# Performance work log

Hardware: AMD Instinct MI355X
Metric: run time of the kernel (lower is better)

## Reference

```python
import jax, jax.numpy as jnp
from jax import lax
import numpy as np

FL = 7      # filter_length (odd so each decomposition level preserves L)
LEVEL = 3
T = 5       # time_points
C = 64      # channels
HID = 64    # ODE hidden width (== C so ODE state shape is preserved)
TD = 16     # time embedding dim
REG = 0.01  # DyWAN reg_factor


def _gelu(x):
    return jax.nn.gelu(x, approximate=False)  # torch nn.GELU default = exact


def _conv1d(x, w, b, pad):
    # x [B,Cin,L], w [Cout,Cin,K] -> [B,Cout,L'] (cross-correlation, as torch)
    out = lax.conv_general_dilated(x, w, (1,), [(pad, pad)],
                                   dimension_numbers=('NCH', 'OIH', 'NCH'))
    return out + b[None, :, None]


def _dywan(x, w1, b1, wg1, bg1, wg2, bg2):
    # DyWAN_Pro: global stats -> dynamic lo/hi filters + regularizers
    stat = x.mean(-1)                                  # AdaptiveAvgPool1d(1)+Flatten
    h = _gelu(stat @ w1.T + b1)
    h = _gelu(h @ wg1.T + bg1)
    f = h @ wg2.T + bg2                                # [B, 2*FL]
    lo, hi = f[:, :FL], f[:, FL:]
    # smoothness: conv1d with kernel [-1,1], zero pad 1 -> xp[l+1]-xp[l]
    lp = jnp.pad(lo, ((0, 0), (1, 1)))
    lo_smooth = jnp.abs(lp[:, 1:] - lp[:, :-1]).mean()
    lo_n = lo / (jnp.linalg.norm(lo, axis=1, keepdims=True) + 1e-8)
    shift_loss = 0.0
    for s in (1, 2, 3):
        sh = jnp.roll(lo_n, s, axis=1)
        shift_loss = shift_loss + jnp.abs(lo_n[:, :, None] * sh[:, None, :]).mean()
    amp_loss = jnp.abs((lo_n ** 2).sum(1) - 1.0).mean()
    ortho = REG * (shift_loss + amp_loss)
    return lo, hi, ortho + lo_smooth * 0.1


def _batch_filter_conv(ap, filt):
    # per-sample depthwise conv: ap [B,C,L], filt [B,FL] -> [B,C,L]
    B, Ch, L = ap.shape
    pad = (FL - 1) // 2
    xp = jnp.pad(ap, ((0, 0), (0, 0), (pad, pad)), mode='edge')  # replicate pad
    xp = xp.reshape(1, B * Ch, L + 2 * pad)
    k = jnp.repeat(filt[:, None, :], Ch, axis=1).reshape(B * Ch, 1, FL)
    out = lax.conv_general_dilated(xp, k, (1,), 'VALID',
                                   dimension_numbers=('NCH', 'OIH', 'NCH'),
                                   feature_group_count=B * Ch)
    return out.reshape(B, Ch, -1)[..., :L]


def _adaptive_time_grid(sig):
    g = jnp.abs(jnp.diff(sig, axis=-1))                          # [B,C,L-1]
    gp = jnp.pad(g, ((0, 0), (0, 0), (2, 2)))                    # avg_pool1d k=5 pad=2
    cs = jnp.pad(jnp.cumsum(gp, axis=-1), ((0, 0), (0, 0), (1, 0)))
    inten = (cs[..., 5:] - cs[..., :-5]) / 5.0                   # [B,C,L-1]
    mn, mx = inten.min(), inten.max()
    td = jnp.where(mx - mn < 1e-8, 0.5,
                   (inten - mn) / (mx - mn + 1e-30) * 0.9 + 0.1)
    tg = jnp.concatenate([jnp.zeros_like(td[..., :1]),
                          jnp.cumsum(td[..., :-1], -1)], -1)     # time_grid
    tg = tg / jnp.maximum(tg.max(), 1e-12)
    idx = np.linspace(0, td.shape[-1] - 1, T).astype(np.int64)   # static indices
    return tg[..., idx].mean((0, 1))                             # [T], increasing


def reference(x, dy_w1, dy_b1, dy_wg1, dy_bg1, dy_wg2, dy_bg2,
              ode_c1w, ode_c1b, ode_c2w, ode_c2b, ode_wt, ode_bt,
              ode_wm, ode_bm, ode_emb,
              gate_w, gate_b, attn1_w, attn1_b, attn2_w, attn2_b):
    # ---- multi-level dynamic wavelet decomposition ----
    coeffs = [x]
    approx = x
    ortho = jnp.float32(0.0)
    for _ in range(LEVEL):
        lo, hi, ortho = _dywan(approx, dy_w1, dy_b1, dy_wg1, dy_bg1, dy_wg2, dy_bg2)
        new_approx = _batch_filter_conv(approx, lo)
        detail = _batch_filter_conv(approx, hi)
        coeffs.append(detail)
        approx = new_approx
    coeffs[0] = approx

    # ---- per-scale ODE evolution: RK4 over the adaptive time grid ----
    def ode_f(t, y, lvl):
        h = _conv1d(y, ode_c1w[lvl], ode_c1b[lvl], 1)
        h = _gelu(h)
        h = _conv1d(h, ode_c2w[lvl], ode_c2b[lvl], 1)
        temb = jax.nn.silu(ode_wt[lvl][:, 0] * t + ode_bt[lvl])   # [TD]
        gb = ode_wm[lvl] @ temb + ode_bm[lvl]                     # [2*HID]
        gamma, beta = gb[:HID], gb[HID:]
        se = ode_emb[lvl, lvl]                                    # scale embedding
        mod = h * (1.0 + gamma + se)[None, :, None] + beta[None, :, None]
        return jax.nn.silu(mod) - 0.1 * y                         # PhysicsActivation

    evolved = []
    for lvl in range(LEVEL + 1):
        c = coeffs[lvl]
        ts = _adaptive_time_grid(c)
        y = c
        for j in range(T - 1):
            t0, t1 = ts[j], ts[j + 1]
            dt = t1 - t0
            k1 = ode_f(t0, y, lvl)
            k2 = ode_f(t0 + dt / 2, y + dt / 2 * k1, lvl)
            k3 = ode_f(t0 + dt / 2, y + dt / 2 * k2, lvl)
            k4 = ode_f(t1, y + dt * k3, lvl)
            y = y + dt / 6 * (k1 + 2 * k2 + 2 * k3 + k4)
        e_in = jnp.mean(c ** 2, axis=(1, 2), keepdims=True)
        e_out = jnp.mean(y ** 2, axis=(1, 2), keepdims=True)
        evolved.append(y * jnp.sqrt(e_in / (e_out + 1e-8)))       # energy constraint

    # ---- gated cross-scale fusion ----
    current = evolved[0]
    yh = evolved[1:]
    enhanced = []
    for i in range(LEVEL - 1, -1, -1):
        detail = yh[i]
        if i < LEVEL - 1:
            a = _gelu(_conv1d(current, attn1_w[i], attn1_b[i], 0))
            a = jax.nn.sigmoid(_conv1d(a, attn2_w[i], attn2_b[i], 0))
            detail = detail * a + detail
        gate = jax.nn.sigmoid(_conv1d(current, gate_w[i], gate_b[i], 1))
        current = current + gate * detail
        enhanced.append(detail)
    enhanced.reverse()
    out = jnp.stack([current] + enhanced, axis=0)   # [LEVEL+1, B, C, L] = (yl, yh...)
    return out, ortho


def setup_inputs() -> dict:
    key = jax.random.key(0)
    ks = jax.random.split(key, 16)
    B, L = 8, 2048

    def rn(k, shape, sc=0.1):
        return jax.random.normal(k, shape, dtype=jnp.float32) * sc

    return {
        'x': jax.random.normal(ks[0], (B, C, L), dtype=jnp.float32),
        'dy_w1': rn(ks[1], (HID, C)),
        'dy_b1': jnp.zeros((HID,), jnp.float32),
        'dy_wg1': rn(ks[2], (2 * HID, HID)),
        'dy_bg1': jnp.zeros((2 * HID,), jnp.float32),
        'dy_wg2': rn(ks[3], (2 * FL, 2 * HID)),
        'dy_bg2': rn(ks[4], (2 * FL,), 0.1),
        'ode_c1w': rn(ks[5], (LEVEL + 1, HID, C, 3)),
        'ode_c1b': jnp.zeros((LEVEL + 1, HID), jnp.float32),
        'ode_c2w': rn(ks[6], (LEVEL + 1, HID, HID, 3)),
        'ode_c2b': jnp.zeros((LEVEL + 1, HID), jnp.float32),
        'ode_wt': rn(ks[7], (LEVEL + 1, TD, 1)),
        'ode_bt': jnp.zeros((LEVEL + 1, TD), jnp.float32),
        'ode_wm': rn(ks[8], (LEVEL + 1, 2 * HID, TD)),
        'ode_bm': jnp.zeros((LEVEL + 1, 2 * HID), jnp.float32),
        'ode_emb': rn(ks[9], (LEVEL + 1, 8, HID)),
        'gate_w': rn(ks[10], (LEVEL, C, C, 3)),
        'gate_b': jnp.zeros((LEVEL, C), jnp.float32),
        'attn1_w': rn(ks[11], (LEVEL - 1, C // 4, C, 1)),
        'attn1_b': jnp.zeros((LEVEL - 1, C // 4), jnp.float32),
        'attn2_w': rn(ks[12], (LEVEL - 1, C, C // 4, 1)),
        'attn2_b': jnp.zeros((LEVEL - 1, C), jnp.float32),
    }
```

## Files before the change

### kernel.cpp

```cpp
#include <hip/hip_runtime.h>
#include <math.h>

#define LSEQ 2048
#define NB 8
#define NCH 64
#define NTOT (NB*NCH*LSEQ)
#define NROWS (NB*NCH)

typedef __attribute__((ext_vector_type(8))) short short8;
typedef __attribute__((ext_vector_type(4))) float float4v;

__device__ __forceinline__ float geluf(float x){
    return 0.5f*x*(1.0f+erff(x*0.70710678118654752f));
}
__device__ __forceinline__ float siluf(float x){
    return x/(1.0f+expf(-x));
}
__device__ __forceinline__ float sigf(float x){
    return 1.0f/(1.0f+expf(-x));
}
__device__ __forceinline__ unsigned short f2bf(float f){
    unsigned u=__float_as_uint(f);
    u += 0x7fffu + ((u>>16)&1u);
    return (unsigned short)(u>>16);
}
__device__ __forceinline__ float bf2f(unsigned h){
    return __uint_as_float((h&0xffffu)<<16);
}

__global__ __launch_bounds__(256) void wtrans_kernel(const float* __restrict__ w,
                                                     float* __restrict__ wt){
    int idx = blockIdx.x*256 + threadIdx.x;
    int j = idx >> 6, co = idx & 63;
    wt[idx] = w[co*192 + j];
}

__global__ __launch_bounds__(256) void wprep_kernel(const float* __restrict__ c1w,
                                                    const float* __restrict__ c2w,
                                                    short* __restrict__ WB){
    int idx = blockIdx.x*256 + threadIdx.x;
    if (idx >= 196608) return;
    int ci  = idx & 63;
    int co  = (idx>>6) & 63;
    int tap = (idx>>12) % 3;
    int st  = (idx/(3<<12)) & 1;
    int lvl = idx/(6<<12);
    const float* src = (st==0? c1w : c2w);
    float w = src[(size_t)lvl*12288 + co*192 + ci*3 + tap];
    unsigned short hi = f2bf(w);
    float lo = w - bf2f(hi);
    size_t base = ((((size_t)(lvl*2+st)*2+0)*3+tap)*64+co)*64+ci;
    size_t basl = ((((size_t)(lvl*2+st)*2+1)*3+tap)*64+co)*64+ci;
    WB[base] = (short)hi;
    WB[basl] = (short)f2bf(lo);
}

__global__ __launch_bounds__(256) void stat_kernel(const float* __restrict__ in,
                                                   float* __restrict__ stat){
    int r = blockIdx.x, tid = threadIdx.x;
    const float* p = in + (size_t)r*LSEQ;
    float acc = 0.f;
    for (int i=tid;i<LSEQ;i+=256) acc += p[i];
    for (int o=32;o>0;o>>=1) acc += __shfl_down(acc,o,64);
    __shared__ float red[4];
    if ((tid&63)==0) red[tid>>6]=acc;
    __syncthreads();
    if (tid==0) stat[r] = (red[0]+red[1]+red[2]+red[3])*(1.0f/LSEQ);
}

__global__ __launch_bounds__(256) void dywan_kernel(
    const float* __restrict__ stat,
    const float* __restrict__ w1, const float* __restrict__ b1,
    const float* __restrict__ wg1, const float* __restrict__ bg1,
    const float* __restrict__ wg2, const float* __restrict__ bg2,
    float* __restrict__ lo_out, float* __restrict__ hi_out,
    float* __restrict__ ortho_out)
{
    __shared__ float st[512];
    __shared__ float h1s[512];
    __shared__ float h2s[1024];
    __shared__ float fs[112];
    int tid = threadIdx.x;
    for (int i=tid;i<512;i+=256) st[i]=stat[i];
    __syncthreads();
    for (int idx=tid; idx<512; idx+=256){
        int b=idx>>6, j=idx&63;
        float acc=b1[j];
        const float* W=w1+j*64;
        for (int i=0;i<64;i++) acc += st[b*64+i]*W[i];
        h1s[idx]=geluf(acc);
    }
    __syncthreads();
    for (int idx=tid; idx<1024; idx+=256){
        int b=idx>>7, j=idx&127;
        float acc=bg1[j];
        const float* W=wg1+j*64;
        for (int i=0;i<64;i++) acc += h1s[b*64+i]*W[i];
        h2s[idx]=geluf(acc);
    }
    __syncthreads();
    if (tid<112){
        int b=tid/14, j=tid-b*14;
        float acc=bg2[j];
        const float* W=wg2+j*128;
        for (int i=0;i<128;i++) acc += h2s[b*128+i]*W[i];
        fs[tid]=acc;
    }
    __syncthreads();
    if (tid<56){
        int b=tid/7, k=tid-b*7;
        lo_out[tid]=fs[b*14+k];
        hi_out[tid]=fs[b*14+7+k];
    }
    if (tid==0){
        float smooth=0.f, shiftsum=0.f, ampsum=0.f;
        for (int b=0;b<8;b++){
            const float* l = fs + b*14;
            float prev=0.f, nrm=0.f;
            for (int k=0;k<7;k++){ smooth += fabsf(l[k]-prev); prev=l[k]; nrm += l[k]*l[k]; }
            smooth += fabsf(prev);
            float denom = sqrtf(nrm) + 1e-8f;
            float sabs=0.f, s2=0.f;
            for (int k=0;k<7;k++){ float v=l[k]/denom; sabs+=fabsf(v); s2+=v*v; }
            shiftsum += sabs*sabs;
            ampsum += fabsf(s2-1.0f);
        }
        smooth *= (1.0f/64.0f);
        float shift = 3.0f*shiftsum/(8.0f*49.0f);
        float amp = ampsum*(1.0f/8.0f);
        *ortho_out = 0.01f*(shift+amp) + 0.1f*smooth;
    }
}

__global__ __launch_bounds__(256) void filt_kernel(
    const float* __restrict__ ap, const float* __restrict__ lo,
    const float* __restrict__ hi, float* __restrict__ na,
    float* __restrict__ det)
{
    int r = blockIdx.y, l0 = blockIdx.x*256, tid = threadIdx.x;
    int b = r>>6;
    __shared__ float s[262];
    __shared__ float fl[7], fh[7];
    for (int idx=tid; idx<262; idx+=256){
        int l = l0+idx-3;
        l = min(max(l,0),LSEQ-1);
        s[idx]=ap[(size_t)r*LSEQ+l];
    }
    if (tid<7) fl[tid]=lo[b*7+tid];
    else if (tid<14) fh[tid-7]=hi[b*7+tid-7];
    __syncthreads();
    float a=0.f, d=0.f;
    #pragma unroll
    for (int k=0;k<7;k++){ float v=s[tid+k]; a+=v*fl[k]; d+=v*fh[k]; }
    na[(size_t)r*LSEQ+l0+tid]=a;
    det[(size_t)r*LSEQ+l0+tid]=d;
}

__global__ __launch_bounds__(256) void tg_pass1(const float* __restrict__ CB,
                                                float* __restrict__ rowstats){
    __shared__ float sh[2048];
    __shared__ float red[28];
    int r = blockIdx.x, lvl = blockIdx.y, tid = threadIdx.x;
    const float* s = CB + (size_t)lvl*NTOT + (size_t)r*LSEQ;
    float* rso = rowstats + (size_t)(lvl*NROWS+r)*8;
    for (int i=tid;i<2048;i+=256) sh[i]=s[i];
    __syncthreads();
    float ssq=0.f;
    for (int i=tid;i<2048;i+=256){ float v=sh[i]; ssq+=v*v; }
    float mn=1e30f, mx=-1e30f, s0=0.f,s1=0.f,s2=0.f,s3=0.f;
    for (int j=tid;j<2047;j+=256){
        int k0 = (j-2>0)? j-2:0;
        int k1 = (j+2<2046)? j+2:2046;
        float acc=0.f;
        for (int k=k0;k<=k1;k++) acc += fabsf(sh[k+1]-sh[k]);
        float inten = acc*0.2f;
        mn=fminf(mn,inten); mx=fmaxf(mx,inten);
        if (j<511)  s0+=inten;
        if (j<1023) s1+=inten;
        if (j<1534) s2+=inten;
        if (j<2046) s3+=inten;
    }
    float vals[7]={mn,mx,s0,s1,s2,s3,ssq};
    for (int o=32;o>0;o>>=1){
        vals[0]=fminf(vals[0],__shfl_down(vals[0],o,64));
        vals[1]=fmaxf(vals[1],__shfl_down(vals[1],o,64));
        vals[2]+=__shfl_down(vals[2],o,64);
        vals[3]+=__shfl_down(vals[3],o,64);
        vals[4]+=__shfl_down(vals[4],o,64);
        vals[5]+=__shfl_down(vals[5],o,64);
        vals[6]+=__shfl_down(vals[6],o,64);
    }
    int lane=tid&63, w=tid>>6;
    if (lane==0) for (int q=0;q<7;q++) red[w*7+q]=vals[q];
    __syncthreads();
    if (tid==0){
        rso[0]=fminf(fminf(red[0],red[7]),fminf(red[14],red[21]));
        rso[1]=fmaxf(fmaxf(red[1],red[8]),fmaxf(red[15],red[22]));
        rso[2]=red[2]+red[9]+red[16]+red[23];
        rso[3]=red[3]+red[10]+red[17]+red[24];
        rso[4]=red[4]+red[11]+red[18]+red[25];
        rso[5]=red[5]+red[12]+red[19]+red[26];
        rso[6]=red[6]+red[13]+red[20]+red[27];
    }
}

__global__ __launch_bounds__(256) void tg_finalize(
    const float* __restrict__ rowstats,
    const float* __restrict__ wt, const float* __restrict__ bt,
    const float* __restrict__ wm, const float* __restrict__ bm,
    const float* __restrict__ emb,
    float* __restrict__ ts_out, float* __restrict__ modsc,
    float* __restrict__ modbi, float* __restrict__ ein,
    float* __restrict__ eout)
{
    int tid=threadIdx.x;
    const int lvl=blockIdx.x;
    const float* rs = rowstats + (size_t)lvl*NROWS*8;
    __shared__ float red[28];
    __shared__ float stv[9];
    __shared__ float temb[144];
    float mn=1e30f,mx=-1e30f,a0=0.f,a1=0.f,a2=0.f,a3=0.f,m3=-1e30f;
    for (int r=tid;r<512;r+=256){
        mn=fminf(mn,rs[r*8+0]); mx=fmaxf(mx,rs[r*8+1]);
        a0+=rs[r*8+2]; a1+=rs[r*8+3]; a2+=rs[r*8+4]; a3+=rs[r*8+5];
        m3=fmaxf(m3,rs[r*8+5]);
    }
    float vals[7]={mn,mx,a0,a1,a2,a3,m3};
    for (int o=32;o>0;o>>=1){
        vals[0]=fminf(vals[0],__shfl_down(vals[0],o,64));
        vals[1]=fmaxf(vals[1],__shfl_down(vals[1],o,64));
        vals[2]+=__shfl_down(vals[2],o,64);
        vals[3]+=__shfl_down(vals[3],o,64);
        vals[4]+=__shfl_down(vals[4],o,64);
        vals[5]+=__shfl_down(vals[5],o,64);
        vals[6]=fmaxf(vals[6],__shfl_down(vals[6],o,64));
    }
    int lane=tid&63, w=tid>>6;
    if (lane==0) for (int q=0;q<7;q++) red[w*7+q]=vals[q];
    if (tid<8){
        float e=0.f;
        for (int c=0;c<64;c++) e += rs[(tid*64+c)*8+6];
        ein[lvl*8+tid]=e*(1.0f/131072.0f);
        eout[lvl*8+tid]=0.f;
    }
    __syncthreads();
    if (tid==0){
        float mnv=fminf(fminf(red[0],red[7]),fminf(red[14],red[21]));
        float mxv=fmaxf(fmaxf(red[1],red[8]),fmaxf(red[15],red[22]));
        float s0=red[2]+red[9]+red[16]+red[23];
        float s1=red[3]+red[10]+red[17]+red[24];
        float s2=red[4]+red[11]+red[18]+red[25];
        float s3=red[5]+red[12]+red[19]+red[26];
        float m3v=fmaxf(fmaxf(red[6],red[13]),fmaxf(red[20],red[27]));
        const float idxs[5]={0.f,511.f,1023.f,1534.f,2046.f};
        float tsv[5];
        if (mxv-mnv < 1e-8f){
            for (int k=0;k<5;k++) tsv[k]=idxs[k]/2046.0f;
        } else {
            float a = 0.9f/(mxv-mnv+1e-30f);
            float bb = 0.1f - a*mnv;
            float gmax = a*m3v + bb*2046.0f;
            float sums[5]={0.f,s0,s1,s2,s3};
            tsv[0]=0.f;
            for (int k=1;k<5;k++)
                tsv[k]=(a*(sums[k]*(1.0f/512.0f)) + bb*idxs[k])/gmax;
        }
        for (int k=0;k<5;k++){ ts_out[lvl*8+k]=tsv[k]; stv[2*k]=tsv[k]; }
        for (int k=0;k<4;k++) stv[2*k+1]=tsv[k] + 0.5f*(tsv[k+1]-tsv[k]);
    }
    __syncthreads();
    if (tid<144){
        int m=tid>>4, i=tid&15;
        float z = wt[lvl*16+i]*stv[m] + bt[lvl*16+i];
        temb[tid]=siluf(z);
    }
    __syncthreads();
    for (int idx=tid; idx<1152; idx+=256){
        int m=idx>>7, c=idx&127;
        float g=bm[lvl*128+c];
        const float* W=wm+(size_t)(lvl*128+c)*16;
        const float* te=temb+m*16;
        for (int i=0;i<16;i++) g += W[i]*te[i];
        if (c<64) modsc[lvl*576+m*64+c]=1.0f+g+emb[(lvl*8+lvl)*64+c];
        else      modbi[lvl*576+m*64+(c-64)]=g;
    }
}

__global__ __launch_bounds__(256) void ode_eval_all(
    const float* __restrict__ yinB, const unsigned* __restrict__ kprevB,
    unsigned* __restrict__ koutB, unsigned* __restrict__ accB,
    float* __restrict__ youtB,
    const short* __restrict__ WB, const float* __restrict__ c1bB,
    const float* __restrict__ c2bB,
    const float* __restrict__ modscB, const float* __restrict__ modbiB,
    const float* __restrict__ tsB, float* __restrict__ eoutB,
    int step, int eval, int do_energy)
{
    __shared__ unsigned yTh[68][36];
    __shared__ unsigned yTl[68][36];
    __shared__ unsigned hTh[66][36];
    __shared__ float red[4];
    const int tid=threadIdx.x;
    const int lvl=blockIdx.z;
    const int b=blockIdx.y;
    const int l0=blockIdx.x*64;
    const size_t loff=(size_t)lvl*NTOT;
    const size_t loffP=(size_t)lvl*(NTOT/2);
    const float* yin = yinB + loff;
    const unsigned* kprev = kprevB + loffP;
    unsigned* kout = koutB + loffP;
    unsigned* acc = accB + loffP;
    float* yout = youtB + loff;
    const float dt = tsB[lvl*8+step+1]-tsB[lvl*8+step];
    const float alpha=(eval==0)?0.f:((eval==3)?dt:0.5f*dt);
    const int tslot=2*step+((eval==0)?0:((eval==3)?2:1));
    const int wv=tid>>6, lane=tid&63;
    const int n=lane&15, quad=lane>>4;
    const int m0=wv*16;

    #pragma unroll
    for (int pass=0; pass<2; pass++){
        int r = pass*64 + lane;
        if (r < 68){
            int l = l0 - 2 + r;
            bool ok = (l>=0 && l<LSEQ);
            #pragma unroll
            for (int qq=0; qq<8; qq++){
                int q = wv*8 + qq;
                float v0=0.f, v1=0.f;
                if (ok){
                    size_t g0=(size_t)(b*64+2*q)*LSEQ+l;
                    v0=yin[g0]; v1=yin[g0+LSEQ];
                    if (eval!=0){
                        unsigned ku = kprev[((size_t)(b*32+q))*LSEQ + l];
                        v0 += alpha*bf2f(ku);
                        v1 += alpha*bf2f(ku>>16);
                    }
                }
                unsigned short h0=f2bf(v0), h1=f2bf(v1);
                yTh[r][q] = (unsigned)h0 | ((unsigned)h1<<16);
                yTl[r][q] = (unsigned)f2bf(v0-bf2f(h0)) | ((unsigned)f2bf(v1-bf2f(h1))<<16);
            }
        }
    }
    __syncthreads();

    {
        const short* W1 = WB + (size_t)(lvl*2+0)*2*3*4096;
        short8 A[3][2][2];
        #pragma unroll
        for (int tap=0;tap<3;tap++)
            #pragma unroll
            for (int ks=0;ks<2;ks++)
                #pragma unroll
                for (int hl=0;hl<2;hl++)
                    A[tap][ks][hl] = *(const short8*)(W1 + (((size_t)hl*3+tap)*64 + (m0+n))*64 + ks*32 + quad*8);
        float bia[4];
        #pragma unroll
        for (int reg=0;reg<4;reg++) bia[reg]=c1bB[lvl*64 + m0 + quad*4 + reg];
        const int q0=(m0>>1)+quad*2;
        for (int nt=0; nt<5; nt++){
            float4v d = {bia[0],bia[1],bia[2],bia[3]};
            #pragma unroll
            for (int tap=0;tap<3;tap++){
                int rr = 16*nt + n + tap;
                rr = (rr>67)? 67 : rr;
                const unsigned* ph=&yTh[rr][0];
                const unsigned* pl=&yTl[rr][0];
                #pragma unroll
                for (int ks=0;ks<2;ks++){
                    short8 bh = *(const short8*)(ph + ks*16 + quad*4);
                    short8 bl = *(const short8*)(pl + ks*16 + quad*4);
                    d = __builtin_amdgcn_mfma_f32_16x16x32_bf16(A[tap][ks][0], bh, d, 0,0,0);
                    d = __builtin_amdgcn_mfma_f32_16x16x32_bf16(A[tap][ks][0], bl, d, 0,0,0);
                    d = __builtin_amdgcn_mfma_f32_16x16x32_bf16(A[tap][ks][1], bh, d, 0,0,0);
                }
            }
            if (nt<4 || n<2){
                int rh = 16*nt + n;
                int hpos = l0 - 1 + rh;
                bool okh = (hpos>=0 && hpos<LSEQ);
                float h0 = okh? geluf(d[0]) : 0.f;
                float h1 = okh? geluf(d[1]) : 0.f;
                float h2 = okh? geluf(d[2]) : 0.f;
                float h3 = okh? geluf(d[3]) : 0.f;
                hTh[rh][q0]   = (unsigned)f2bf(h0) | ((unsigned)f2bf(h1)<<16);
                hTh[rh][q0+1] = (unsigned)f2bf(h2) | ((unsigned)f2bf(h3)<<16);
            }
        }
    }
    __syncthreads();

    float esum=0.f;
    {
        const short* W2 = WB + (size_t)(lvl*2+1)*2*3*4096;
        short8 A[3][2][2];
        #pragma unroll
        for (int tap=0;tap<3;tap++)
            #pragma unroll
            for (int ks=0;ks<2;ks++)
                #pragma unroll
                for (int hl=0;hl<2;hl++)
                    A[tap][ks][hl] = *(const short8*)(W2 + (((size_t)hl*3+tap)*64 + (m0+n))*64 + ks*32 + quad*8);
        float bib[4], sc[4], bi2[4];
        #pragma unroll
        for (int reg=0;reg<4;reg++){
            int co = m0 + quad*4 + reg;
            bib[reg]=c2bB[lvl*64+co];
            sc[reg]=modscB[lvl*576+tslot*64+co];
            bi2[reg]=modbiB[lvl*576+tslot*64+co];
        }
        const float dt6 = dt/6.0f;
        const int qy0=(m0+quad*4)>>1;
        for (int nt=0; nt<4; nt++){
            float4v d = {bib[0],bib[1],bib[2],bib[3]};
            #pragma unroll
            for (int tap=0;tap<3;tap++){
                const int rr = 16*nt + n + tap;
                const unsigned* ph=&hTh[rr][0];
                #pragma unroll
                for (int ks=0;ks<2;ks++){
                    short8 bh = *(const short8*)(ph + ks*16 + quad*4);
                    d = __builtin_amdgcn_mfma_f32_16x16x32_bf16(A[tap][ks][0], bh, d, 0,0,0);
                    d = __builtin_amdgcn_mfma_f32_16x16x32_bf16(A[tap][ks][1], bh, d, 0,0,0);
                }
            }
            int p = l0 + 16*nt + n;
            int ry = 16*nt + n + 2;
            unsigned uh0=yTh[ry][qy0],   ul0=yTl[ry][qy0];
            unsigned uh1=yTh[ry][qy0+1], ul1=yTl[ry][qy0+1];
            float yev[4];
            yev[0]=bf2f(uh0)+bf2f(ul0);
            yev[1]=bf2f(uh0>>16)+bf2f(ul0>>16);
            yev[2]=bf2f(uh1)+bf2f(ul1);
            yev[3]=bf2f(uh1>>16)+bf2f(ul1>>16);
            float kv[4];
            #pragma unroll
            for (int reg=0;reg<4;reg++){
                float m = d[reg]*sc[reg] + bi2[reg];
                kv[reg] = siluf(m) - 0.1f*yev[reg];
            }
            size_t ia = ((size_t)(b*32+qy0))*LSEQ + p;
            size_t ib = ia + LSEQ;
            if (eval==0){
                unsigned ka=(unsigned)f2bf(kv[0])|((unsigned)f2bf(kv[1])<<16);
                unsigned kb=(unsigned)f2bf(kv[2])|((unsigned)f2bf(kv[3])<<16);
                kout[ia]=ka; kout[ib]=kb;
                acc[ia]=ka;  acc[ib]=kb;
            } else if (eval<3){
                unsigned ka=(unsigned)f2bf(kv[0])|((unsigned)f2bf(kv[1])<<16);
                unsigned kb=(unsigned)f2bf(kv[2])|((unsigned)f2bf(kv[3])<<16);
                kout[ia]=ka; kout[ib]=kb;
                unsigned ua=acc[ia], ub=acc[ib];
                float a0=bf2f(ua)+2.f*kv[0],     a1=bf2f(ua>>16)+2.f*kv[1];
                float a2=bf2f(ub)+2.f*kv[2],     a3=bf2f(ub>>16)+2.f*kv[3];
                acc[ia]=(unsigned)f2bf(a0)|((unsigned)f2bf(a1)<<16);
                acc[ib]=(unsigned)f2bf(a2)|((unsigned)f2bf(a3)<<16);
            } else {
                unsigned ua=acc[ia], ub=acc[ib];
                float av[4]={bf2f(ua),bf2f(ua>>16),bf2f(ub),bf2f(ub>>16)};
                size_t gbase=(size_t)(b*64 + m0 + quad*4)*LSEQ + p;
                #pragma unroll
                for (int reg=0;reg<4;reg++){
                    size_t gi = gbase + (size_t)reg*LSEQ;
                    float yn = yin[gi] + dt6*(av[reg]+kv[reg]);
                    yout[gi]=yn;
                    esum += yn*yn;
                }
            }
        }
    }
    if (do_energy){
        for (int o=32;o>0;o>>=1) esum+=__shfl_down(esum,o,64);
        if ((tid&63)==0) red[tid>>6]=esum;
        __syncthreads();
        if (tid==0) atomicAdd(&eoutB[lvl*8+b], red[0]+red[1]+red[2]+red[3]);
    }
}

__global__ __launch_bounds__(256) void scale_kernel(
    const float* __restrict__ y, const float* __restrict__ ein,
    const float* __restrict__ eout, float* __restrict__ o)
{
    int idx = blockIdx.x*256 + threadIdx.x;
    int lb = idx>>17;
    float eo = eout[lb]*(1.0f/131072.0f);
    o[idx] = y[idx]*sqrtf(ein[lb]/(eo+1e-8f));
}

__global__ __launch_bounds__(256) void recon_kernel(
    const float* __restrict__ cur, float* __restrict__ detail,
    const float* __restrict__ a1w, const float* __restrict__ a1b,
    const float* __restrict__ a2w, const float* __restrict__ a2b,
    const float* __restrict__ gwt, const float* __restrict__ gb,
    float* __restrict__ curout, int has_attn)
{
    __shared__ float yc[64][66];
    __shared__ float dtile[64][65];
    __shared__ float hid[16][64];
    const int tid=threadIdx.x, b=blockIdx.y, l0=blockIdx.x*64;
    for (int idx=tid; idx<64*66; idx+=256){
        int ci=idx/66, u=idx-ci*66;
        int l=l0+u-1;
        yc[ci][u]=(l>=0 && l<LSEQ)? cur[(size_t)(b*64+ci)*LSEQ+l] : 0.f;
    }
    for (int idx=tid; idx<4096; idx+=256){
        int ci=idx>>6, p=idx&63;
        dtile[ci][p]=detail[(size_t)(b*64+ci)*LSEQ+l0+p];
    }
    __syncthreads();
    if (has_attn){
        for (int idx=tid; idx<1024; idx+=256){
            int h=idx>>6, p=idx&63;
            float acc=a1b[h];
            const float* W=a1w+h*64;
            for (int ci=0;ci<64;ci++) acc += W[ci]*yc[ci][p+1];
            hid[h][p]=geluf(acc);
        }
        __syncthreads();
        for (int idx=tid; idx<4096; idx+=256){
            int co=idx>>6, p=idx&63;
            float acc=a2b[co];
            const float* W=a2w+co*16;
            #pragma unroll
            for (int h=0;h<16;h++) acc += W[h]*hid[h][p];
            float a=sigf(acc);
            float dnew = dtile[co][p]*(1.0f+a);
            dtile[co][p]=dnew;
            detail[(size_t)(b*64+co)*LSEQ+l0+p]=dnew;
        }
        __syncthreads();
    }
    const int co=tid&63, g=tid>>6;
    const int p0=g*16;
    float a[16];
    float bb=gb[co];
    #pragma unroll
    for (int i=0;i<16;i++) a[i]=bb;
    for (int ci=0;ci<64;ci++){
        float w0=gwt[(ci*3+0)*64+co];
        float w1_=gwt[(ci*3+1)*64+co];
        float w2_=gwt[(ci*3+2)*64+co];
        float x[18];
        #pragma unroll
        for (int j=0;j<18;j++) x[j]=yc[ci][p0+j];
        #pragma unroll
        for (int i=0;i<16;i++) a[i] += w0*x[i]+w1_*x[i+1]+w2_*x[i+2];
    }
    float r[16];
    #pragma unroll
    for (int i=0;i<16;i++){
        float gt=sigf(a[i]);
        r[i]=yc[co][p0+i+1]+gt*dtile[co][p0+i];
    }
    __syncthreads();
    #pragma unroll
    for (int i=0;i<16;i++) dtile[co][p0+i]=r[i];
    __syncthreads();
    for (int idx=tid; idx<4096; idx+=256){
        int ci=idx>>6, p=idx&63;
        curout[(size_t)(b*64+ci)*LSEQ+l0+p]=dtile[ci][p];
    }
}

extern "C" void kernel_launch(void* const* d_in, const int* in_sizes, int n_in,
                              void* d_out, int out_size, void* d_ws, size_t ws_size,
                              hipStream_t stream)
{
    (void)in_sizes; (void)n_in; (void)out_size; (void)ws_size;
    const float* x       =(const float*)d_in[0];
    const float* dy_w1   =(const float*)d_in[1];
    const float* dy_b1   =(const float*)d_in[2];
    const float* dy_wg1  =(const float*)d_in[3];
    const float* dy_bg1  =(const float*)d_in[4];
    const float* dy_wg2  =(const float*)d_in[5];
    const float* dy_bg2  =(const float*)d_in[6];
    const float* ode_c1w =(const float*)d_in[7];
    const float* ode_c1b =(const float*)d_in[8];
    const float* ode_c2w =(const float*)d_in[9];
    const float* ode_c2b =(const float*)d_in[10];
    const float* ode_wt  =(const float*)d_in[11];
    const float* ode_bt  =(const float*)d_in[12];
    const float* ode_wm  =(const float*)d_in[13];
    const float* ode_bm  =(const float*)d_in[14];
    const float* ode_emb =(const float*)d_in[15];
    const float* gate_w  =(const float*)d_in[16];
    const float* gate_b  =(const float*)d_in[17];
    const float* attn1_w =(const float*)d_in[18];
    const float* attn1_b =(const float*)d_in[19];
    const float* attn2_w =(const float*)d_in[20];
    const float* attn2_b =(const float*)d_in[21];
    float* out=(float*)d_out;
    float* ws=(float*)d_ws;
    const size_t N=NTOT;
    float* CB = ws;
    float* PB = ws+4*N;
    float* QB = ws+8*N;
    unsigned* K0P=(unsigned*)(ws+12*N);
    unsigned* K1P=(unsigned*)(ws+14*N);
    unsigned* ACP=(unsigned*)(ws+16*N);
    float* SM = ws+20*N;
    float* stat_ws =SM;
    float* lo_ws   =SM+512;
    float* hi_ws   =SM+576;
    float* rowstats=SM+1024;
    float* ts_ws   =SM+17408;
    float* modsc   =SM+17536;
    float* modbi   =SM+19840;
    float* ein     =SM+22144;
    float* eoutb   =SM+22176;
    short* WB      =(short*)(SM+24576);
    float* WTG     =SM+24576+196608;

    dim3 blk(256);

    wprep_kernel<<<768,blk,0,stream>>>(ode_c1w, ode_c2w, WB);
    for (int i=0;i<3;i++)
        wtrans_kernel<<<48,blk,0,stream>>>(gate_w+(size_t)i*12288, WTG+(size_t)i*12288);

    const float* cura=x;
    float* outsA[3]={PB, PB+N, CB};
    float* outsD[3]={CB+N, CB+2*N, CB+3*N};
    for (int lv=0; lv<3; lv++){
        stat_kernel<<<NROWS,blk,0,stream>>>(cura, stat_ws);
        dywan_kernel<<<1,blk,0,stream>>>(stat_ws, dy_w1,dy_b1,dy_wg1,dy_bg1,dy_wg2,dy_bg2,
                                         lo_ws, hi_ws, out+4*N);
        filt_kernel<<<dim3(8,NROWS),blk,0,stream>>>(cura, lo_ws, hi_ws, outsA[lv], outsD[lv]);
        cura=outsA[lv];
    }

    tg_pass1<<<dim3(NROWS,4),blk,0,stream>>>(CB, rowstats);
    tg_finalize<<<4,blk,0,stream>>>(rowstats, ode_wt, ode_bt, ode_wm, ode_bm,
                                    ode_emb, ts_ws, modsc, modbi, ein, eoutb);

    const float* yins[4]={CB, PB, QB, PB};
    float*       youts[4]={PB, QB, PB, QB};
    for (int step=0;step<4;step++){
        for (int ev=0;ev<4;ev++){
            const unsigned* kp=(ev==2)? K1P : K0P;
            unsigned* ko=(ev==1)? K1P : K0P;
            int doe=(step==3 && ev==3)?1:0;
            ode_eval_all<<<dim3(32,NB,4),blk,0,stream>>>(
                yins[step],kp,ko,ACP,youts[step],
                WB,ode_c1b,ode_c2b,modsc,modbi,ts_ws,eoutb,step,ev,doe);
        }
    }
    scale_kernel<<<4*NTOT/256,blk,0,stream>>>(QB, ein, eoutb, out);

    recon_kernel<<<dim3(32,NB),blk,0,stream>>>(out+0*N, out+3*N,
        attn1_w, attn1_b, attn2_w, attn2_b,
        WTG+2*12288, gate_b+128, PB, 0);
    recon_kernel<<<dim3(32,NB),blk,0,stream>>>(PB, out+2*N,
        attn1_w+1024, attn1_b+16, attn2_w+1024, attn2_b+64,
        WTG+1*12288, gate_b+64, QB, 1);
    recon_kernel<<<dim3(32,NB),blk,0,stream>>>(QB, out+1*N,
        attn1_w, attn1_b, attn2_w, attn2_b,
        WTG, gate_b, out+0*N, 1);
}
```

Measured before the change: 751.4 us.

## Fuse row-mean stats into filter kernel and energy scaling into recon

The per-level stat kernel launches are removed. The next level's row means are built by a block reduction plus atomicAdd inside filt_kernel, and dywan_kernel divides by LSEQ and zeroes the accumulator after reading it. The standalone scale kernel is also dropped. recon_kernel now applies the per-level energy-rescale factor while loading the ODE outputs and detail bands from QB, and writes the scaled details to the output. This saves one full read/write pass over four levels of data plus several launches, at the cost of atomics and extra store loops in recon.

```diff
diff --git a/kernel.cpp b/kernel.cpp
--- a/kernel.cpp
+++ b/kernel.cpp
@@ -65,11 +65,11 @@
     __shared__ float red[4];
     if ((tid&63)==0) red[tid>>6]=acc;
     __syncthreads();
-    if (tid==0) stat[r] = (red[0]+red[1]+red[2]+red[3])*(1.0f/LSEQ);
+    if (tid==0) stat[r] = red[0]+red[1]+red[2]+red[3];
 }
 
 __global__ __launch_bounds__(256) void dywan_kernel(
-    const float* __restrict__ stat,
+    float* __restrict__ stat,
     const float* __restrict__ w1, const float* __restrict__ b1,
     const float* __restrict__ wg1, const float* __restrict__ bg1,
     const float* __restrict__ wg2, const float* __restrict__ bg2,
@@ -81,8 +81,9 @@
     __shared__ float h2s[1024];
     __shared__ float fs[112];
     int tid = threadIdx.x;
-    for (int i=tid;i<512;i+=256) st[i]=stat[i];
-    __syncthreads();
+    for (int i=tid;i<512;i+=256) st[i]=stat[i]*(1.0f/LSEQ);
+    __syncthreads();
+    for (int i=tid;i<512;i+=256) stat[i]=0.f;
     for (int idx=tid; idx<512; idx+=256){
         int b=idx>>6, j=idx&63;
         float acc=b1[j];
@@ -135,12 +136,13 @@
 __global__ __launch_bounds__(256) void filt_kernel(
     const float* __restrict__ ap, const float* __restrict__ lo,
     const float* __restrict__ hi, float* __restrict__ na,
-    float* __restrict__ det)
+    float* __restrict__ det, float* __restrict__ stat_out)
 {
     int r = blockIdx.y, l0 = blockIdx.x*256, tid = threadIdx.x;
     int b = r>>6;
     __shared__ float s[262];
     __shared__ float fl[7], fh[7];
+    __shared__ float sred[4];
     for (int idx=tid; idx<262; idx+=256){
         int l = l0+idx-3;
         l = min(max(l,0),LSEQ-1);
@@ -154,6 +156,13 @@
     for (int k=0;k<7;k++){ float v=s[tid+k]; a+=v*fl[k]; d+=v*fh[k]; }
     na[(size_t)r*LSEQ+l0+tid]=a;
     det[(size_t)r*LSEQ+l0+tid]=d;
+    if (stat_out){
+        float sm=a;
+        for (int o=32;o>0;o>>=1) sm += __shfl_down(sm,o,64);
+        if ((tid&63)==0) sred[tid>>6]=sm;
+        __syncthreads();
+        if (tid==0) atomicAdd(&stat_out[r], sred[0]+sred[1]+sred[2]+sred[3]);
+    }
 }
 
 __global__ __launch_bounds__(256) void tg_pass1(const float* __restrict__ CB,
@@ -478,35 +487,37 @@
     }
 }
 
-__global__ __launch_bounds__(256) void scale_kernel(
-    const float* __restrict__ y, const float* __restrict__ ein,
-    const float* __restrict__ eout, float* __restrict__ o)
-{
-    int idx = blockIdx.x*256 + threadIdx.x;
-    int lb = idx>>17;
-    float eo = eout[lb]*(1.0f/131072.0f);
-    o[idx] = y[idx]*sqrtf(ein[lb]/(eo+1e-8f));
-}
-
 __global__ __launch_bounds__(256) void recon_kernel(
-    const float* __restrict__ cur, float* __restrict__ detail,
+    const float* __restrict__ cur, const float* __restrict__ det_in,
+    float* __restrict__ det_out,
     const float* __restrict__ a1w, const float* __restrict__ a1b,
     const float* __restrict__ a2w, const float* __restrict__ a2b,
     const float* __restrict__ gwt, const float* __restrict__ gb,
-    float* __restrict__ curout, int has_attn)
+    float* __restrict__ curout,
+    const float* __restrict__ ein, const float* __restrict__ eout,
+    int lvl_cur, int lvl_det, int has_attn)
 {
     __shared__ float yc[64][66];
     __shared__ float dtile[64][65];
     __shared__ float hid[16][64];
     const int tid=threadIdx.x, b=blockIdx.y, l0=blockIdx.x*64;
+    float scur=1.f, sdet;
+    if (lvl_cur>=0){
+        float eo=eout[lvl_cur*8+b]*(1.0f/131072.0f);
+        scur=sqrtf(ein[lvl_cur*8+b]/(eo+1e-8f));
+    }
+    {
+        float eo=eout[lvl_det*8+b]*(1.0f/131072.0f);
+        sdet=sqrtf(ein[lvl_det*8+b]/(eo+1e-8f));
+    }
     for (int idx=tid; idx<64*66; idx+=256){
         int ci=idx/66, u=idx-ci*66;
         int l=l0+u-1;
-        yc[ci][u]=(l>=0 && l<LSEQ)? cur[(size_t)(b*64+ci)*LSEQ+l] : 0.f;
+        yc[ci][u]=(l>=0 && l<LSEQ)? scur*cur[(size_t)(b*64+ci)*LSEQ+l] : 0.f;
     }
     for (int idx=tid; idx<4096; idx+=256){
         int ci=idx>>6, p=idx&63;
-        dtile[ci][p]=detail[(size_t)(b*64+ci)*LSEQ+l0+p];
+        dtile[ci][p]=sdet*det_in[(size_t)(b*64+ci)*LSEQ+l0+p];
     }
     __syncthreads();
     if (has_attn){
@@ -527,9 +538,14 @@
             float a=sigf(acc);
             float dnew = dtile[co][p]*(1.0f+a);
             dtile[co][p]=dnew;
-            detail[(size_t)(b*64+co)*LSEQ+l0+p]=dnew;
+            det_out[(size_t)(b*64+co)*LSEQ+l0+p]=dnew;
         }
         __syncthreads();
+    } else {
+        for (int idx=tid; idx<4096; idx+=256){
+            int ci=idx>>6, p=idx&63;
+            det_out[(size_t)(b*64+ci)*LSEQ+l0+p]=dtile[ci][p];
+        }
     }
     const int co=tid&63, g=tid>>6;
     const int p0=g*16;
@@ -618,14 +634,16 @@
     for (int i=0;i<3;i++)
         wtrans_kernel<<<48,blk,0,stream>>>(gate_w+(size_t)i*12288, WTG+(size_t)i*12288);
 
+    stat_kernel<<<NROWS,blk,0,stream>>>(x, stat_ws);
     const float* cura=x;
     float* outsA[3]={PB, PB+N, CB};
     float* outsD[3]={CB+N, CB+2*N, CB+3*N};
     for (int lv=0; lv<3; lv++){
-        stat_kernel<<<NROWS,blk,0,stream>>>(cura, stat_ws);
         dywan_kernel<<<1,blk,0,stream>>>(stat_ws, dy_w1,dy_b1,dy_wg1,dy_bg1,dy_wg2,dy_bg2,
                                          lo_ws, hi_ws, out+4*N);
-        filt_kernel<<<dim3(8,NROWS),blk,0,stream>>>(cura, lo_ws, hi_ws, outsA[lv], outsD[lv]);
+        float* statn = (lv<2)? stat_ws : nullptr;
+        filt_kernel<<<dim3(8,NROWS),blk,0,stream>>>(cura, lo_ws, hi_ws,
+                                                    outsA[lv], outsD[lv], statn);
         cura=outsA[lv];
     }
 
@@ -645,15 +663,14 @@
                 WB,ode_c1b,ode_c2b,modsc,modbi,ts_ws,eoutb,step,ev,doe);
         }
     }
-    scale_kernel<<<4*NTOT/256,blk,0,stream>>>(QB, ein, eoutb, out);
-
-    recon_kernel<<<dim3(32,NB),blk,0,stream>>>(out+0*N, out+3*N,
+
+    recon_kernel<<<dim3(32,NB),blk,0,stream>>>(QB+0*N, QB+3*N, out+3*N,
         attn1_w, attn1_b, attn2_w, attn2_b,
-        WTG+2*12288, gate_b+128, PB, 0);
-    recon_kernel<<<dim3(32,NB),blk,0,stream>>>(PB, out+2*N,
+        WTG+2*12288, gate_b+128, PB, ein, eoutb, 0, 3, 0);
+    recon_kernel<<<dim3(32,NB),blk,0,stream>>>(PB, QB+2*N, out+2*N,
         attn1_w+1024, attn1_b+16, attn2_w+1024, attn2_b+64,
-        WTG+1*12288, gate_b+64, QB, 1);
-    recon_kernel<<<dim3(32,NB),blk,0,stream>>>(QB, out+1*N,
+        WTG+1*12288, gate_b+64, QB, ein, eoutb, -1, 2, 1);
+    recon_kernel<<<dim3(32,NB),blk,0,stream>>>(QB, QB+1*N, out+1*N,
         attn1_w, attn1_b, attn2_w, attn2_b,
-        WTG, gate_b, out+0*N, 1);
-}
+        WTG, gate_b, out+0*N, ein, eoutb, -1, 1, 1);
+}
```

After: 751.2 us. Within noise of the previous version (-0.0%).
